# Kernel optimization log

Measured on AMD Instinct MI355X. Metric: run time of the kernel, lower is better.

Reference implementation:

```python
import jax, jax.numpy as jnp
import numpy as np

N_RET, N_ORIG, N_EDGE = 200000, 100000, 800000
D_FEAT, HIDDEN, OUT = 128, 128, 64


def _gcn(x_src, ridx, cidx, n_src, n_dst, W, b):
    # GCNConv (add_self_loops=False), bipartite symmetric normalization:
    # norm_e = deg_src[row]^-1/2 * deg_dst[col]^-1/2
    h = x_src @ W                                            # [n_src, H]
    ones = jnp.ones(ridx.shape[0], h.dtype)
    deg_s = jax.ops.segment_sum(ones, ridx, num_segments=n_src)
    deg_d = jax.ops.segment_sum(ones, cidx, num_segments=n_dst)
    inv_s = jnp.where(deg_s > 0, jax.lax.rsqrt(jnp.maximum(deg_s, 1.0)), 0.0)
    inv_d = jnp.where(deg_d > 0, jax.lax.rsqrt(jnp.maximum(deg_d, 1.0)), 0.0)
    norm = inv_s[ridx] * inv_d[cidx]                         # [E]
    out = jax.ops.segment_sum(h[ridx] * norm[:, None], cidx, num_segments=n_dst)
    return out + b


def _sage(x_src, x_dst, sidx, didx, n_dst, Wl, bl, Wr):
    # SAGEConv: mean-aggregate raw src features, then lin_l(agg)+bias + lin_r(x_dst)
    deg = jax.ops.segment_sum(jnp.ones(sidx.shape[0], x_src.dtype), didx, num_segments=n_dst)
    agg = jax.ops.segment_sum(x_src[sidx], didx, num_segments=n_dst)
    agg = agg / jnp.maximum(deg, 1.0)[:, None]
    return agg @ Wl + bl + x_dst @ Wr


def setup_inputs() -> dict:
    key = jax.random.key(0)
    ks = jax.random.split(key, 20)
    def w(k, fan_in, shape):
        return jax.random.normal(k, shape, jnp.float32) / np.sqrt(fan_in)
    inp = {
        "x_ret": jax.random.normal(ks[0], (N_RET, D_FEAT), jnp.float32),
        "x_orig": jax.random.normal(ks[1], (N_ORIG, D_FEAT), jnp.float32),
        "ret_idx": jax.random.randint(ks[2], (N_EDGE,), 0, N_RET, jnp.int32),
        "orig_idx": jax.random.randint(ks[3], (N_EDGE,), 0, N_ORIG, jnp.int32),
        # layer 1 (lazy in = D_FEAT)
        "W_g1": w(ks[4], D_FEAT, (D_FEAT, HIDDEN)), "b_g1": jnp.zeros((HIDDEN,), jnp.float32),
        "Wl1": w(ks[5], D_FEAT, (D_FEAT, HIDDEN)), "bl1": jnp.zeros((HIDDEN,), jnp.float32),
        "Wr1": w(ks[6], D_FEAT, (D_FEAT, HIDDEN)),
        # layer 2 (in = HIDDEN)
        "W_g2": w(ks[7], HIDDEN, (HIDDEN, HIDDEN)), "b_g2": jnp.zeros((HIDDEN,), jnp.float32),
        "Wl2": w(ks[8], HIDDEN, (HIDDEN, HIDDEN)), "bl2": jnp.zeros((HIDDEN,), jnp.float32),
        "Wr2": w(ks[9], HIDDEN, (HIDDEN, HIDDEN)),
        # final linear
        "W_out": w(ks[10], HIDDEN, (HIDDEN, OUT)), "b_out": jnp.zeros((OUT,), jnp.float32),
    }
    return inp


def reference(x_ret, x_orig, ret_idx, orig_idx,
              W_g1, b_g1, Wl1, bl1, Wr1,
              W_g2, b_g2, Wl2, bl2, Wr2,
              W_out, b_out):
    # layer 1: HeteroConv over two relations, then relu per node type
    o1 = jax.nn.relu(_gcn(x_ret, ret_idx, orig_idx, N_RET, N_ORIG, W_g1, b_g1))
    r1 = jax.nn.relu(_sage(x_orig, x_ret, orig_idx, ret_idx, N_RET, Wl1, bl1, Wr1))
    # layer 2
    o2 = jax.nn.relu(_gcn(r1, ret_idx, orig_idx, N_RET, N_ORIG, W_g2, b_g2))
    r2 = jax.nn.relu(_sage(o1, r1, orig_idx, ret_idx, N_RET, Wl2, bl2, Wr2))
    # final linear readout (original code indexes x_dict['author'], which is absent
    # after HeteroConv; we read out the 'original_tweet' node type)
    return o2 @ W_out + b_out
```

## Files before the change

kernel.cpp:

```cpp
#include <hip/hip_runtime.h>

#define N_RET  200000
#define N_ORIG 100000
#define N_EDGE 800000
#define NB_RET  ((N_RET  + 511) >> 9)
#define NB_ORIG ((N_ORIG + 511) >> 9)
#define ECHUNK  2048
#define NCHUNK  ((N_EDGE + ECHUNK - 1) / ECHUNK)
#define NBLK_HO ((N_ORIG + 63) / 64)
#define NBLK_XR ((N_RET + 63) / 64)

typedef __attribute__((ext_vector_type(8))) short bf16x8;
typedef __attribute__((ext_vector_type(4))) float f32x4;

__device__ __forceinline__ ushort f2bf(float f) {
    union { float f; unsigned u; } v; v.f = f;
    unsigned r = v.u + 0x7FFFu + ((v.u >> 16) & 1u);
    return (ushort)(r >> 16);
}
__device__ __forceinline__ float bf2f(ushort u) {
    union { unsigned u; float f; } v; v.u = ((unsigned)u) << 16;
    return v.f;
}
__device__ __forceinline__ int swz(int byteoff) {
    return byteoff ^ ((byteoff >> 4) & 0x70);
}

__global__ void prep_kernel(const float* __restrict__ Wl1, const float* __restrict__ Wr1,
                            const float* __restrict__ Wg2, const float* __restrict__ Wout,
                            ushort* __restrict__ wtl1, ushort* __restrict__ wtr1,
                            ushort* __restrict__ wtg2, ushort* __restrict__ wto,
                            int* __restrict__ bcnt) {
    const int b = blockIdx.x, t = threadIdx.x;
    if (b == 224) {
        for (int i = t; i < 1024; i += 256) bcnt[i] = 0;
        return;
    }
    const float* W; ushort* WT; int base, nshift;
    if (b < 64)       { W = Wl1;  WT = wtl1; base = b;       nshift = 7; }
    else if (b < 128) { W = Wr1;  WT = wtr1; base = b - 64;  nshift = 7; }
    else if (b < 192) { W = Wg2;  WT = wtg2; base = b - 128; nshift = 7; }
    else              { W = Wout; WT = wto;  base = b - 192; nshift = 6; }
    int i = base * 256 + t;
    int k = i >> nshift, n = i & ((1 << nshift) - 1);
    WT[n * 128 + k] = f2bf(W[i]);
}

__global__ __launch_bounds__(256) void bucket_count(const int* __restrict__ ridx,
                                                    const int* __restrict__ cidx,
                                                    int* __restrict__ bcnt1,
                                                    int* __restrict__ bcnt2) {
    __shared__ int h1[512], h2[512];
    const int t = threadIdx.x;
    const int c0 = blockIdx.x * ECHUNK;
    for (int i = t; i < 512; i += 256) { h1[i] = 0; h2[i] = 0; }
    __syncthreads();
    for (int i = t; i < ECHUNK; i += 256) {
        int e = c0 + i;
        if (e < N_EDGE) {
            atomicAdd(&h1[ridx[e] >> 9], 1);
            atomicAdd(&h2[cidx[e] >> 9], 1);
        }
    }
    __syncthreads();
    for (int b = t; b < NB_RET; b += 256)
        if (h1[b]) atomicAdd(&bcnt1[b], h1[b]);
    for (int b = t; b < NB_ORIG; b += 256)
        if (h2[b]) atomicAdd(&bcnt2[b], h2[b]);
}

__global__ __launch_bounds__(256) void scan_buckets(const int* __restrict__ bcnt1,
                                                    int* __restrict__ boff1, int* __restrict__ bcur1,
                                                    const int* __restrict__ bcnt2,
                                                    int* __restrict__ boff2, int* __restrict__ bcur2,
                                                    int* __restrict__ off_ret,
                                                    int* __restrict__ off_orig) {
    __shared__ int sm[256];
    const int t = threadIdx.x;
    {
        int a0 = (2 * t     < NB_RET) ? bcnt1[2 * t]     : 0;
        int a1 = (2 * t + 1 < NB_RET) ? bcnt1[2 * t + 1] : 0;
        sm[t] = a0 + a1;
        __syncthreads();
        for (int d = 1; d < 256; d <<= 1) {
            int v = (t >= d) ? sm[t - d] : 0;
            __syncthreads(); sm[t] += v; __syncthreads();
        }
        int tb = t ? sm[t - 1] : 0;
        if (2 * t < NB_RET)     { boff1[2 * t]     = tb;      bcur1[2 * t]     = tb; }
        if (2 * t + 1 < NB_RET) { boff1[2 * t + 1] = tb + a0; bcur1[2 * t + 1] = tb + a0; }
        if (t == 0) { boff1[NB_RET] = N_EDGE; off_ret[N_RET] = N_EDGE; }
        __syncthreads();
    }
    {
        int a0 = (2 * t     < NB_ORIG) ? bcnt2[2 * t]     : 0;
        int a1 = (2 * t + 1 < NB_ORIG) ? bcnt2[2 * t + 1] : 0;
        sm[t] = a0 + a1;
        __syncthreads();
        for (int d = 1; d < 256; d <<= 1) {
            int v = (t >= d) ? sm[t - d] : 0;
            __syncthreads(); sm[t] += v; __syncthreads();
        }
        int tb = t ? sm[t - 1] : 0;
        if (2 * t < NB_ORIG)     { boff2[2 * t]     = tb;      bcur2[2 * t]     = tb; }
        if (2 * t + 1 < NB_ORIG) { boff2[2 * t + 1] = tb + a0; bcur2[2 * t + 1] = tb + a0; }
        if (t == 0) { boff2[NB_ORIG] = N_EDGE; off_orig[N_ORIG] = N_EDGE; }
    }
}

__global__ __launch_bounds__(256) void bin_both(const int* __restrict__ ridx,
                                                const int* __restrict__ cidx,
                                                int* __restrict__ bcur1, int* __restrict__ bcur2,
                                                int* __restrict__ binned1, int* __restrict__ binned2) {
    __shared__ int hist[512], base[512], lcur[512];
    const int t = threadIdx.x;
    const bool second = blockIdx.x >= NCHUNK;
    const int* dst = second ? cidx : ridx;
    const int* src = second ? ridx : cidx;
    int* bcur = second ? bcur2 : bcur1;
    int* binned = second ? binned2 : binned1;
    const int nbuckets = second ? NB_ORIG : NB_RET;
    const int c0 = (second ? blockIdx.x - NCHUNK : blockIdx.x) * ECHUNK;
    for (int i = t; i < 512; i += 256) { hist[i] = 0; lcur[i] = 0; }
    __syncthreads();
    for (int i = t; i < ECHUNK; i += 256) {
        int e = c0 + i;
        if (e < N_EDGE) atomicAdd(&hist[dst[e] >> 9], 1);
    }
    __syncthreads();
    for (int b = t; b < nbuckets; b += 256)
        base[b] = hist[b] > 0 ? atomicAdd(&bcur[b], hist[b]) : 0;
    __syncthreads();
    for (int i = t; i < ECHUNK; i += 256) {
        int e = c0 + i;
        if (e < N_EDGE) {
            int d = dst[e];
            int b = d >> 9;
            int r = atomicAdd(&lcur[b], 1);
            binned[base[b] + r] = ((d & 511) << 18) | src[e];
        }
    }
}

__global__ __launch_bounds__(256) void fill_both(const int* __restrict__ binned1,
                                                 const int* __restrict__ boff1,
                                                 int* __restrict__ off_ret, int* __restrict__ el1,
                                                 const int* __restrict__ binned2,
                                                 const int* __restrict__ boff2,
                                                 int* __restrict__ off_orig, int* __restrict__ el2) {
    __shared__ int hist[512];
    __shared__ int sm[256];
    const int t = threadIdx.x;
    const bool second = blockIdx.x >= NB_RET;
    const int bkt = second ? blockIdx.x - NB_RET : blockIdx.x;
    const int* binned = second ? binned2 : binned1;
    const int* boff = second ? boff2 : boff1;
    int* off = second ? off_orig : off_ret;
    int* el  = second ? el2 : el1;
    const int nnodes = second ? N_ORIG : N_RET;
    const int base = bkt << 9;
    const int nvalid = min(512, nnodes - base);
    const int s0 = boff[bkt], s1 = boff[bkt + 1];
    for (int i = t; i < 512; i += 256) hist[i] = 0;
    __syncthreads();
    for (int i = s0 + t; i < s1; i += 256)
        atomicAdd(&hist[binned[i] >> 18], 1);
    __syncthreads();
    int a0 = hist[2 * t], a1 = hist[2 * t + 1];
    sm[t] = a0 + a1;
    __syncthreads();
    for (int d = 1; d < 256; d <<= 1) {
        int v = (t >= d) ? sm[t - d] : 0;
        __syncthreads(); sm[t] += v; __syncthreads();
    }
    int tb = (t ? sm[t - 1] : 0) + s0;
    if (2 * t < nvalid)     off[base + 2 * t]     = tb;
    if (2 * t + 1 < nvalid) off[base + 2 * t + 1] = tb + a0;
    hist[2 * t] = tb;
    hist[2 * t + 1] = tb + a0;
    __syncthreads();
    for (int i = s0 + t; i < s1; i += 256) {
        int v = binned[i];
        int p = atomicAdd(&hist[v >> 18], 1);
        el[p] = v & 0x3FFFF;
    }
}

__global__ __launch_bounds__(256) void gemm_lin(const float* __restrict__ Ao,
                                                const float* __restrict__ Ar,
                                                const ushort* __restrict__ WTl,
                                                const ushort* __restrict__ WTr,
                                                ushort* __restrict__ hoB,
                                                ushort* __restrict__ xrB) {
    __shared__ ushort Wlds[128 * 128];
    const int t = threadIdx.x;
    const bool second = blockIdx.x >= NBLK_HO;
    const float* A = second ? Ar : Ao;
    const ushort* WT = second ? WTr : WTl;
    ushort* outp = second ? xrB : hoB;
    const int M = second ? N_RET : N_ORIG;
    const int i0 = (second ? blockIdx.x - NBLK_HO : blockIdx.x) * 64;

    #pragma unroll
    for (int it = 0; it < 8; ++it) {
        int idx = t + 256 * it;
        int n = idx >> 4, u = idx & 15;
        *(bf16x8*)&Wlds[swz(n * 256 + u * 16) >> 1] = *(const bf16x8*)&WT[idx * 8];
    }

    const int w = t >> 6, l = t & 63;
    const int r16 = l & 15, kg = l >> 4;
    const int arow = min(i0 + 16 * w + r16, M - 1);

    float4 v[8];
    #pragma unroll
    for (int j = 0; j < 8; ++j)
        v[j] = *(const float4*)&A[(size_t)arow * 128 + (j >> 1) * 32 + kg * 8 + (j & 1) * 4];
    bf16x8 a[4];
    #pragma unroll
    for (int ks = 0; ks < 4; ++ks) {
        float4 v0 = v[2 * ks], v1 = v[2 * ks + 1];
        bf16x8 f;
        f[0] = (short)f2bf(v0.x); f[1] = (short)f2bf(v0.y);
        f[2] = (short)f2bf(v0.z); f[3] = (short)f2bf(v0.w);
        f[4] = (short)f2bf(v1.x); f[5] = (short)f2bf(v1.y);
        f[6] = (short)f2bf(v1.z); f[7] = (short)f2bf(v1.w);
        a[ks] = f;
    }
    __syncthreads();

    f32x4 acc[8];
    #pragma unroll
    for (int cf = 0; cf < 8; ++cf) acc[cf] = (f32x4){0.f, 0.f, 0.f, 0.f};
    #pragma unroll
    for (int cf = 0; cf < 8; ++cf) {
        int n = cf * 16 + r16;
        #pragma unroll
        for (int ks = 0; ks < 4; ++ks) {
            bf16x8 b = *(const bf16x8*)&Wlds[swz(n * 256 + kg * 16 + ks * 64) >> 1];
            acc[cf] = __builtin_amdgcn_mfma_f32_16x16x32_bf16(a[ks], b, acc[cf], 0, 0, 0);
        }
    }
    __syncthreads();

    #pragma unroll
    for (int r = 0; r < 4; ++r) {
        int row = 16 * w + 4 * kg + r;
        #pragma unroll
        for (int cf = 0; cf < 8; ++cf) {
            int ad = row * 256 + (cf * 16 + r16) * 2;
            Wlds[swz(ad) >> 1] = f2bf(acc[cf][r]);
        }
    }
    __syncthreads();

    const size_t obase = (size_t)i0 * 128;
    #pragma unroll
    for (int j = 0; j < 4; ++j) {
        int lb = j * 4096 + t * 16;
        bf16x8 val = *(const bf16x8*)&Wlds[swz(lb) >> 1];
        if (i0 + (lb >> 8) < M)
            *(bf16x8*)&outp[obase + (lb >> 1)] = val;
    }
}

__global__ void gather_sage(const ushort* __restrict__ ho, const ushort* __restrict__ xr,
                            const int* __restrict__ off, const int* __restrict__ slist,
                            const float* __restrict__ bl, ushort* __restrict__ r1s) {
    int gt = blockIdx.x * 256 + threadIdx.x;
    int node = gt >> 4;
    if (node >= N_RET) return;
    int o8 = gt & 15;
    int s = off[node], e = off[node + 1];
    float acc[8] = {0.f, 0.f, 0.f, 0.f, 0.f, 0.f, 0.f, 0.f};
    for (int i = s; i < e; ++i) {
        int sn = slist[i];
        bf16x8 v = *(const bf16x8*)&ho[(size_t)sn * 128 + o8 * 8];
        #pragma unroll
        for (int j = 0; j < 8; ++j) acc[j] += bf2f((ushort)v[j]);
    }
    int deg = e - s;
    float rinv = 1.0f / fmaxf((float)deg, 1.0f);
    float sinv = deg > 0 ? rsqrtf((float)deg) : 0.f;
    bf16x8 xv = *(const bf16x8*)&xr[(size_t)node * 128 + o8 * 8];
    bf16x8 ov;
    #pragma unroll
    for (int j = 0; j < 8; ++j) {
        float v = fmaxf(acc[j] * rinv + bf2f((ushort)xv[j]) + bl[o8 * 8 + j], 0.f) * sinv;
        ov[j] = (short)f2bf(v);
    }
    *(bf16x8*)&r1s[(size_t)node * 128 + o8 * 8] = ov;
}

__global__ void gather_sum(const ushort* __restrict__ src,
                           const int* __restrict__ off, const int* __restrict__ slist,
                           ushort* __restrict__ dst) {
    int gt = blockIdx.x * 256 + threadIdx.x;
    int node = gt >> 4;
    if (node >= N_ORIG) return;
    int o8 = gt & 15;
    int s = off[node], e = off[node + 1];
    float acc[8] = {0.f, 0.f, 0.f, 0.f, 0.f, 0.f, 0.f, 0.f};
    for (int i = s; i < e; ++i) {
        int sn = slist[i];
        bf16x8 v = *(const bf16x8*)&src[(size_t)sn * 128 + o8 * 8];
        #pragma unroll
        for (int j = 0; j < 8; ++j) acc[j] += bf2f((ushort)v[j]);
    }
    bf16x8 ov;
    #pragma unroll
    for (int j = 0; j < 8; ++j) ov[j] = (short)f2bf(acc[j]);
    *(bf16x8*)&dst[(size_t)node * 128 + o8 * 8] = ov;
}

__global__ __launch_bounds__(256) void gemm_t_out(
    const ushort* __restrict__ g, const ushort* __restrict__ WTg,
    const ushort* __restrict__ WTo, const int* __restrict__ off,
    const float* __restrict__ bg, const float* __restrict__ bo,
    float* __restrict__ out, int M) {
    __shared__ ushort Alds[64 * 128];
    __shared__ ushort Wlds[128 * 128];
    const int t = threadIdx.x;
    const int i0 = blockIdx.x * 64;

    #pragma unroll
    for (int it = 0; it < 8; ++it) {
        int idx = t + 256 * it;
        int n = idx >> 4, u = idx & 15;
        *(bf16x8*)&Wlds[swz(n * 256 + u * 16) >> 1] = *(const bf16x8*)&WTg[idx * 8];
    }
    #pragma unroll
    for (int it = 0; it < 4; ++it) {
        int idx = t + 256 * it;
        int row = idx >> 4, u = idx & 15;
        int gr = min(i0 + row, M - 1);
        bf16x8 v = *(const bf16x8*)&g[(size_t)gr * 128 + u * 8];
        *(bf16x8*)&Alds[swz(row * 256 + u * 16) >> 1] = v;
    }
    __syncthreads();

    const int w = t >> 6, l = t & 63;
    const int r16 = l & 15, kg = l >> 4;
    const int arow = 16 * w + r16;

    bf16x8 a[4];
    #pragma unroll
    for (int ks = 0; ks < 4; ++ks)
        a[ks] = *(const bf16x8*)&Alds[swz(arow * 256 + kg * 16 + ks * 64) >> 1];
    f32x4 acc[8];
    #pragma unroll
    for (int cf = 0; cf < 8; ++cf) acc[cf] = (f32x4){0.f, 0.f, 0.f, 0.f};
    #pragma unroll
    for (int cf = 0; cf < 8; ++cf) {
        int n = cf * 16 + r16;
        #pragma unroll
        for (int ks = 0; ks < 4; ++ks) {
            bf16x8 b = *(const bf16x8*)&Wlds[swz(n * 256 + kg * 16 + ks * 64) >> 1];
            acc[cf] = __builtin_amdgcn_mfma_f32_16x16x32_bf16(a[ks], b, acc[cf], 0, 0, 0);
        }
    }
    __syncthreads();

    #pragma unroll
    for (int r = 0; r < 4; ++r) {
        int row = 16 * w + 4 * kg + r;
        int grc = min(i0 + row, M - 1);
        int dg = off[grc + 1] - off[grc];
        float di = dg > 0 ? rsqrtf((float)dg) : 0.f;
        #pragma unroll
        for (int cf = 0; cf < 8; ++cf) {
            int col = cf * 16 + r16;
            float v = fmaxf(acc[cf][r] * di + bg[col], 0.f);
            Alds[swz(row * 256 + col * 2) >> 1] = f2bf(v);
        }
    }
    #pragma unroll
    for (int it = 0; it < 4; ++it) {
        int idx = t + 256 * it;
        int n = idx >> 4, u = idx & 15;
        *(bf16x8*)&Wlds[swz(n * 256 + u * 16) >> 1] = *(const bf16x8*)&WTo[idx * 8];
    }
    __syncthreads();

    bf16x8 a2[4];
    #pragma unroll
    for (int ks = 0; ks < 4; ++ks)
        a2[ks] = *(const bf16x8*)&Alds[swz(arow * 256 + kg * 16 + ks * 64) >> 1];
    f32x4 acc2[4];
    #pragma unroll
    for (int cf = 0; cf < 4; ++cf) acc2[cf] = (f32x4){0.f, 0.f, 0.f, 0.f};
    #pragma unroll
    for (int cf = 0; cf < 4; ++cf) {
        int n = cf * 16 + r16;
        #pragma unroll
        for (int ks = 0; ks < 4; ++ks) {
            bf16x8 b = *(const bf16x8*)&Wlds[swz(n * 256 + kg * 16 + ks * 64) >> 1];
            acc2[cf] = __builtin_amdgcn_mfma_f32_16x16x32_bf16(a2[ks], b, acc2[cf], 0, 0, 0);
        }
    }
    #pragma unroll
    for (int r = 0; r < 4; ++r) {
        int gr = i0 + 16 * w + 4 * kg + r;
        if (gr >= M) continue;
        #pragma unroll
        for (int cf = 0; cf < 4; ++cf) {
            int col = cf * 16 + r16;
            out[(size_t)gr * 64 + col] = acc2[cf][r] + bo[col];
        }
    }
}

extern "C" void kernel_launch(void* const* d_in, const int* in_sizes, int n_in,
                              void* d_out, int out_size, void* d_ws, size_t ws_size,
                              hipStream_t stream) {
    const float* x_ret    = (const float*)d_in[0];
    const float* x_orig   = (const float*)d_in[1];
    const int*   ret_idx  = (const int*)d_in[2];
    const int*   orig_idx = (const int*)d_in[3];
    const float* Wl1  = (const float*)d_in[6];
    const float* bl1  = (const float*)d_in[7];
    const float* Wr1  = (const float*)d_in[8];
    const float* Wg2  = (const float*)d_in[9];
    const float* bg2  = (const float*)d_in[10];
    const float* Wout = (const float*)d_in[14];
    const float* bout = (const float*)d_in[15];
    float* out = (float*)d_out;

    ushort* hoB  = (ushort*)d_ws;
    ushort* xrB  = hoB + (size_t)N_ORIG * 128;
    ushort* r1sB = xrB + (size_t)N_RET * 128;
    ushort* wtl1 = r1sB + (size_t)N_RET * 128;
    ushort* wtr1 = wtl1 + 16384;
    ushort* wtg2 = wtr1 + 16384;
    ushort* wto  = wtg2 + 16384;
    int* off_ret  = (int*)(wto + 8192);
    int* off_orig = off_ret + N_RET + 1;
    int* bcnt1    = off_orig + N_ORIG + 1;
    int* bcnt2    = bcnt1 + 512;
    int* boff1    = bcnt2 + 512;
    int* boff2    = boff1 + 512;
    int* bcur1    = boff2 + 512;
    int* bcur2    = bcur1 + 512;
    int* el1      = bcur2 + 512;
    int* el2      = el1 + N_EDGE;
    int* binned1  = el2 + N_EDGE;
    int* binned2  = binned1 + N_EDGE;

    prep_kernel<<<225, 256, 0, stream>>>(Wl1, Wr1, Wg2, Wout, wtl1, wtr1, wtg2, wto, bcnt1);

    bucket_count<<<NCHUNK, 256, 0, stream>>>(ret_idx, orig_idx, bcnt1, bcnt2);
    scan_buckets<<<1, 256, 0, stream>>>(bcnt1, boff1, bcur1, bcnt2, boff2, bcur2,
                                        off_ret, off_orig);
    bin_both<<<2 * NCHUNK, 256, 0, stream>>>(ret_idx, orig_idx, bcur1, bcur2, binned1, binned2);
    fill_both<<<NB_RET + NB_ORIG, 256, 0, stream>>>(binned1, boff1, off_ret, el1,
                                                    binned2, boff2, off_orig, el2);

    gemm_lin<<<NBLK_HO + NBLK_XR, 256, 0, stream>>>(
        x_orig, x_ret, wtl1, wtr1, hoB, xrB);

    gather_sage<<<(N_RET * 16) / 256, 256, 0, stream>>>(hoB, xrB, off_ret, el1, bl1, r1sB);

    gather_sum<<<(N_ORIG * 16) / 256, 256, 0, stream>>>(r1sB, off_orig, el2, hoB);

    gemm_t_out<<<(N_ORIG + 63) / 64, 256, 0, stream>>>(hoB, wtg2, wto, off_orig,
                                                       bg2, bout, out, N_ORIG);
}
```

Baseline: 217.9 us.

## Merge weight prep with bucket count, fill with GEMM, unroll gathers by two

Weight transpose/convert and edge bucket counting now run in one launch, with bucket counters cleared by a memset instead of a dedicated block. The CSR fill blocks and the first-layer linear GEMM blocks share one launch through a single shared-memory buffer, so the independent GEMM work can overlap the fill. Both gather loops process two edges per iteration to put more loads in flight. This removes two kernel launches and their idle tails, but adds a memset call and a heterogeneous grid whose block types differ in shared-memory use.

```diff
diff --git a/kernel.cpp b/kernel.cpp
--- a/kernel.cpp
+++ b/kernel.cpp
@@ -5,6 +5,7 @@
 #define N_EDGE 800000
 #define NB_RET  ((N_RET  + 511) >> 9)
 #define NB_ORIG ((N_ORIG + 511) >> 9)
+#define FILLB   (NB_RET + NB_ORIG)
 #define ECHUNK  2048
 #define NCHUNK  ((N_EDGE + ECHUNK - 1) / ECHUNK)
 #define NBLK_HO ((N_ORIG + 63) / 64)
@@ -26,33 +27,27 @@
     return byteoff ^ ((byteoff >> 4) & 0x70);
 }
 
-__global__ void prep_kernel(const float* __restrict__ Wl1, const float* __restrict__ Wr1,
-                            const float* __restrict__ Wg2, const float* __restrict__ Wout,
-                            ushort* __restrict__ wtl1, ushort* __restrict__ wtr1,
-                            ushort* __restrict__ wtg2, ushort* __restrict__ wto,
-                            int* __restrict__ bcnt) {
+__global__ __launch_bounds__(256) void prep_count(
+    const float* __restrict__ Wl1, const float* __restrict__ Wr1,
+    const float* __restrict__ Wg2, const float* __restrict__ Wout,
+    ushort* __restrict__ wtl1, ushort* __restrict__ wtr1,
+    ushort* __restrict__ wtg2, ushort* __restrict__ wto,
+    const int* __restrict__ ridx, const int* __restrict__ cidx,
+    int* __restrict__ bcnt1, int* __restrict__ bcnt2) {
+    __shared__ int h1[512], h2[512];
     const int b = blockIdx.x, t = threadIdx.x;
-    if (b == 224) {
-        for (int i = t; i < 1024; i += 256) bcnt[i] = 0;
+    if (b < 224) {
+        const float* W; ushort* WT; int base, nshift;
+        if (b < 64)       { W = Wl1;  WT = wtl1; base = b;       nshift = 7; }
+        else if (b < 128) { W = Wr1;  WT = wtr1; base = b - 64;  nshift = 7; }
+        else if (b < 192) { W = Wg2;  WT = wtg2; base = b - 128; nshift = 7; }
+        else              { W = Wout; WT = wto;  base = b - 192; nshift = 6; }
+        int i = base * 256 + t;
+        int k = i >> nshift, n = i & ((1 << nshift) - 1);
+        WT[n * 128 + k] = f2bf(W[i]);
         return;
     }
-    const float* W; ushort* WT; int base, nshift;
-    if (b < 64)       { W = Wl1;  WT = wtl1; base = b;       nshift = 7; }
-    else if (b < 128) { W = Wr1;  WT = wtr1; base = b - 64;  nshift = 7; }
-    else if (b < 192) { W = Wg2;  WT = wtg2; base = b - 128; nshift = 7; }
-    else              { W = Wout; WT = wto;  base = b - 192; nshift = 6; }
-    int i = base * 256 + t;
-    int k = i >> nshift, n = i & ((1 << nshift) - 1);
-    WT[n * 128 + k] = f2bf(W[i]);
-}
-
-__global__ __launch_bounds__(256) void bucket_count(const int* __restrict__ ridx,
-                                                    const int* __restrict__ cidx,
-                                                    int* __restrict__ bcnt1,
-                                                    int* __restrict__ bcnt2) {
-    __shared__ int h1[512], h2[512];
-    const int t = threadIdx.x;
-    const int c0 = blockIdx.x * ECHUNK;
+    const int c0 = (b - 224) * ECHUNK;
     for (int i = t; i < 512; i += 256) { h1[i] = 0; h2[i] = 0; }
     __syncthreads();
     for (int i = t; i < ECHUNK; i += 256) {
@@ -63,10 +58,10 @@
         }
     }
     __syncthreads();
-    for (int b = t; b < NB_RET; b += 256)
-        if (h1[b]) atomicAdd(&bcnt1[b], h1[b]);
-    for (int b = t; b < NB_ORIG; b += 256)
-        if (h2[b]) atomicAdd(&bcnt2[b], h2[b]);
+    for (int bb = t; bb < NB_RET; bb += 256)
+        if (h1[bb]) atomicAdd(&bcnt1[bb], h1[bb]);
+    for (int bb = t; bb < NB_ORIG; bb += 256)
+        if (h2[bb]) atomicAdd(&bcnt2[bb], h2[bb]);
 }
 
 __global__ __launch_bounds__(256) void scan_buckets(const int* __restrict__ bcnt1,
@@ -142,64 +137,65 @@
     }
 }
 
-__global__ __launch_bounds__(256) void fill_both(const int* __restrict__ binned1,
-                                                 const int* __restrict__ boff1,
-                                                 int* __restrict__ off_ret, int* __restrict__ el1,
-                                                 const int* __restrict__ binned2,
-                                                 const int* __restrict__ boff2,
-                                                 int* __restrict__ off_orig, int* __restrict__ el2) {
-    __shared__ int hist[512];
-    __shared__ int sm[256];
+__global__ __launch_bounds__(256) void fill_gemm(
+    const int* __restrict__ binned1, const int* __restrict__ boff1,
+    int* __restrict__ off_ret, int* __restrict__ el1,
+    const int* __restrict__ binned2, const int* __restrict__ boff2,
+    int* __restrict__ off_orig, int* __restrict__ el2,
+    const float* __restrict__ Ao, const float* __restrict__ Ar,
+    const ushort* __restrict__ WTl, const ushort* __restrict__ WTr,
+    ushort* __restrict__ hoB, ushort* __restrict__ xrB) {
+    __shared__ char smem[32768];
     const int t = threadIdx.x;
-    const bool second = blockIdx.x >= NB_RET;
-    const int bkt = second ? blockIdx.x - NB_RET : blockIdx.x;
-    const int* binned = second ? binned2 : binned1;
-    const int* boff = second ? boff2 : boff1;
-    int* off = second ? off_orig : off_ret;
-    int* el  = second ? el2 : el1;
-    const int nnodes = second ? N_ORIG : N_RET;
-    const int base = bkt << 9;
-    const int nvalid = min(512, nnodes - base);
-    const int s0 = boff[bkt], s1 = boff[bkt + 1];
-    for (int i = t; i < 512; i += 256) hist[i] = 0;
-    __syncthreads();
-    for (int i = s0 + t; i < s1; i += 256)
-        atomicAdd(&hist[binned[i] >> 18], 1);
-    __syncthreads();
-    int a0 = hist[2 * t], a1 = hist[2 * t + 1];
-    sm[t] = a0 + a1;
-    __syncthreads();
-    for (int d = 1; d < 256; d <<= 1) {
-        int v = (t >= d) ? sm[t - d] : 0;
-        __syncthreads(); sm[t] += v; __syncthreads();
-    }
-    int tb = (t ? sm[t - 1] : 0) + s0;
-    if (2 * t < nvalid)     off[base + 2 * t]     = tb;
-    if (2 * t + 1 < nvalid) off[base + 2 * t + 1] = tb + a0;
-    hist[2 * t] = tb;
-    hist[2 * t + 1] = tb + a0;
-    __syncthreads();
-    for (int i = s0 + t; i < s1; i += 256) {
-        int v = binned[i];
-        int p = atomicAdd(&hist[v >> 18], 1);
-        el[p] = v & 0x3FFFF;
-    }
-}
-
-__global__ __launch_bounds__(256) void gemm_lin(const float* __restrict__ Ao,
-                                                const float* __restrict__ Ar,
-                                                const ushort* __restrict__ WTl,
-                                                const ushort* __restrict__ WTr,
-                                                ushort* __restrict__ hoB,
-                                                ushort* __restrict__ xrB) {
-    __shared__ ushort Wlds[128 * 128];
-    const int t = threadIdx.x;
-    const bool second = blockIdx.x >= NBLK_HO;
+    const int b = blockIdx.x;
+
+    if (b < FILLB) {
+        int* hist = (int*)smem;
+        int* sm   = (int*)(smem + 2048);
+        const bool second = b >= NB_RET;
+        const int bkt = second ? b - NB_RET : b;
+        const int* binned = second ? binned2 : binned1;
+        const int* boff = second ? boff2 : boff1;
+        int* off = second ? off_orig : off_ret;
+        int* el  = second ? el2 : el1;
+        const int nnodes = second ? N_ORIG : N_RET;
+        const int base = bkt << 9;
+        const int nvalid = min(512, nnodes - base);
+        const int s0 = boff[bkt], s1 = boff[bkt + 1];
+        for (int i = t; i < 512; i += 256) hist[i] = 0;
+        __syncthreads();
+        for (int i = s0 + t; i < s1; i += 256)
+            atomicAdd(&hist[binned[i] >> 18], 1);
+        __syncthreads();
+        int a0 = hist[2 * t], a1 = hist[2 * t + 1];
+        sm[t] = a0 + a1;
+        __syncthreads();
+        for (int d = 1; d < 256; d <<= 1) {
+            int v = (t >= d) ? sm[t - d] : 0;
+            __syncthreads(); sm[t] += v; __syncthreads();
+        }
+        int tb = (t ? sm[t - 1] : 0) + s0;
+        if (2 * t < nvalid)     off[base + 2 * t]     = tb;
+        if (2 * t + 1 < nvalid) off[base + 2 * t + 1] = tb + a0;
+        hist[2 * t] = tb;
+        hist[2 * t + 1] = tb + a0;
+        __syncthreads();
+        for (int i = s0 + t; i < s1; i += 256) {
+            int v = binned[i];
+            int p = atomicAdd(&hist[v >> 18], 1);
+            el[p] = v & 0x3FFFF;
+        }
+        return;
+    }
+
+    ushort* Wlds = (ushort*)smem;
+    const int gb = b - FILLB;
+    const bool second = gb >= NBLK_HO;
     const float* A = second ? Ar : Ao;
     const ushort* WT = second ? WTr : WTl;
     ushort* outp = second ? xrB : hoB;
     const int M = second ? N_RET : N_ORIG;
-    const int i0 = (second ? blockIdx.x - NBLK_HO : blockIdx.x) * 64;
+    const int i0 = (second ? gb - NBLK_HO : gb) * 64;
 
     #pragma unroll
     for (int it = 0; it < 8; ++it) {
@@ -237,8 +233,8 @@
         int n = cf * 16 + r16;
         #pragma unroll
         for (int ks = 0; ks < 4; ++ks) {
-            bf16x8 b = *(const bf16x8*)&Wlds[swz(n * 256 + kg * 16 + ks * 64) >> 1];
-            acc[cf] = __builtin_amdgcn_mfma_f32_16x16x32_bf16(a[ks], b, acc[cf], 0, 0, 0);
+            bf16x8 bb = *(const bf16x8*)&Wlds[swz(n * 256 + kg * 16 + ks * 64) >> 1];
+            acc[cf] = __builtin_amdgcn_mfma_f32_16x16x32_bf16(a[ks], bb, acc[cf], 0, 0, 0);
         }
     }
     __syncthreads();
@@ -273,7 +269,16 @@
     int o8 = gt & 15;
     int s = off[node], e = off[node + 1];
     float acc[8] = {0.f, 0.f, 0.f, 0.f, 0.f, 0.f, 0.f, 0.f};
-    for (int i = s; i < e; ++i) {
+    int i = s;
+    for (; i + 2 <= e; i += 2) {
+        int sn0 = slist[i], sn1 = slist[i + 1];
+        bf16x8 v0 = *(const bf16x8*)&ho[(size_t)sn0 * 128 + o8 * 8];
+        bf16x8 v1 = *(const bf16x8*)&ho[(size_t)sn1 * 128 + o8 * 8];
+        #pragma unroll
+        for (int j = 0; j < 8; ++j)
+            acc[j] += bf2f((ushort)v0[j]) + bf2f((ushort)v1[j]);
+    }
+    if (i < e) {
         int sn = slist[i];
         bf16x8 v = *(const bf16x8*)&ho[(size_t)sn * 128 + o8 * 8];
         #pragma unroll
@@ -301,7 +306,16 @@
     int o8 = gt & 15;
     int s = off[node], e = off[node + 1];
     float acc[8] = {0.f, 0.f, 0.f, 0.f, 0.f, 0.f, 0.f, 0.f};
-    for (int i = s; i < e; ++i) {
+    int i = s;
+    for (; i + 2 <= e; i += 2) {
+        int sn0 = slist[i], sn1 = slist[i + 1];
+        bf16x8 v0 = *(const bf16x8*)&src[(size_t)sn0 * 128 + o8 * 8];
+        bf16x8 v1 = *(const bf16x8*)&src[(size_t)sn1 * 128 + o8 * 8];
+        #pragma unroll
+        for (int j = 0; j < 8; ++j)
+            acc[j] += bf2f((ushort)v0[j]) + bf2f((ushort)v1[j]);
+    }
+    if (i < e) {
         int sn = slist[i];
         bf16x8 v = *(const bf16x8*)&src[(size_t)sn * 128 + o8 * 8];
         #pragma unroll
@@ -446,16 +460,18 @@
     int* binned1  = el2 + N_EDGE;
     int* binned2  = binned1 + N_EDGE;
 
-    prep_kernel<<<225, 256, 0, stream>>>(Wl1, Wr1, Wg2, Wout, wtl1, wtr1, wtg2, wto, bcnt1);
-
-    bucket_count<<<NCHUNK, 256, 0, stream>>>(ret_idx, orig_idx, bcnt1, bcnt2);
+    hipMemsetAsync(bcnt1, 0, 1024 * sizeof(int), stream);
+
+    prep_count<<<224 + NCHUNK, 256, 0, stream>>>(Wl1, Wr1, Wg2, Wout,
+                                                 wtl1, wtr1, wtg2, wto,
+                                                 ret_idx, orig_idx, bcnt1, bcnt2);
+
     scan_buckets<<<1, 256, 0, stream>>>(bcnt1, boff1, bcur1, bcnt2, boff2, bcur2,
                                         off_ret, off_orig);
     bin_both<<<2 * NCHUNK, 256, 0, stream>>>(ret_idx, orig_idx, bcur1, bcur2, binned1, binned2);
-    fill_both<<<NB_RET + NB_ORIG, 256, 0, stream>>>(binned1, boff1, off_ret, el1,
-                                                    binned2, boff2, off_orig, el2);
-
-    gemm_lin<<<NBLK_HO + NBLK_XR, 256, 0, stream>>>(
+
+    fill_gemm<<<FILLB + NBLK_HO + NBLK_XR, 256, 0, stream>>>(
+        binned1, boff1, off_ret, el1, binned2, boff2, off_orig, el2,
         x_orig, x_ret, wtl1, wtr1, hoB, xrB);
 
     gather_sage<<<(N_RET * 16) / 256, 256, 0, stream>>>(hoB, xrB, off_ret, el1, bl1, r1sB);
```

New measurement: 207.0 us. 5.0% less time.
